# Performance work log

Hardware: AMD Instinct MI355X
Metric: run time of the kernel (lower is better)

Reference implementation:

```python
import jax, jax.numpy as jnp
import numpy as np

N, C = 32768, 1230   # batch of samples, LVIS-scale class count
P = 0.8              # seesaw scale parameter
EPS = 1e-6


def setup_inputs() -> dict:
    key = jax.random.key(0)
    k1, k2, k3 = jax.random.split(key, 3)
    logits = jax.random.normal(k1, (N, C), dtype=jnp.float32)
    labels = jax.random.randint(k2, (N,), 0, C)
    targets = jax.nn.one_hot(labels, C, dtype=jnp.float32)  # one-hot float targets
    # class_counts: long-tailed per-class sample counts (buffer, built in __init__)
    counts = jax.random.randint(k3, (C,), 1, 100000).astype(jnp.float32)
    cond = counts[:, None] > counts[None, :]
    s = jnp.where(cond, (counts[None, :] / counts[:, None]) ** P,
                  jnp.ones((C, C), dtype=jnp.float32))
    return {"logits": logits, "targets": targets, "s": s}


def reference(logits, targets, s):
    # numerically-stable shift (matches torch: logits - max)
    logits = logits - jnp.max(logits, axis=-1, keepdims=True)
    e = jnp.exp(logits)                                   # [N, C]
    # denom[n,i] = sum_j (1 - t[n,j]) * s[i,j] * e[n,j] + e[n,i]
    # original code materializes [N, C, C]; algebraically this is a GEMM:
    denom = jnp.einsum('nj,ij->ni', (1.0 - targets) * e, s) + e
    sigma = e / (denom + EPS)
    loss = -(targets * jnp.log(sigma)).sum(-1)            # [N]
    return loss.mean()
```

## Files before the change

kernel.cpp:

```cpp
#include <hip/hip_runtime.h>
#include <math.h>


constexpr int N_ROWS = 32768;
constexpr int C_CLS  = 1230;
constexpr int C2     = C_CLS / 2;
constexpr int BLK    = 256;
constexpr int WPB    = BLK / 64;
constexpr int ITERS  = (C2 + 63) / 64;
constexpr float EPS_F = 1e-6f;

__global__ __launch_bounds__(BLK) void seesaw_row_kernel(
    const float* __restrict__ logits,
    const float* __restrict__ targets,
    const float* __restrict__ s,
    float* __restrict__ row_loss)
{
    const int t    = threadIdx.x;
    const int lane = t & 63;
    const int wv   = t >> 6;
    const int n    = blockIdx.x * WPB + wv;

    const float2* lrow = reinterpret_cast<const float2*>(logits  + (size_t)n * C_CLS);
    const float2* trow = reinterpret_cast<const float2*>(targets + (size_t)n * C_CLS);

    float2 l[ITERS];
    float lmax = -INFINITY;
    float lval = 0.0f;
    int   li   = 0;

    #pragma unroll
    for (int it = 0; it < ITERS; ++it) {
        const int j2 = lane + it * 64;
        if (j2 < C2) {
            l[it] = lrow[j2];
            const float2 tv = trow[j2];
            lmax = fmaxf(lmax, fmaxf(l[it].x, l[it].y));
            if (tv.x > 0.5f) { li = 2 * j2;     lval = l[it].x; }
            if (tv.y > 0.5f) { li = 2 * j2 + 1; lval = l[it].y; }
        }
    }
    #pragma unroll
    for (int off = 32; off > 0; off >>= 1) {
        lmax  = fmaxf(lmax, __shfl_xor(lmax, off));
        li   += __shfl_xor(li, off);
        lval += __shfl_xor(lval, off);
    }
    const int   li_u = __builtin_amdgcn_readfirstlane(li);
    const float m    = lmax;

    const float2* srow = reinterpret_cast<const float2*>(s + (size_t)li_u * C_CLS);
    const float sii = s[(size_t)li_u * C_CLS + li_u];

    float part = 0.0f;
    #pragma unroll
    for (int it = 0; it < ITERS; ++it) {
        const int j2 = lane + it * 64;
        if (j2 < C2) {
            const float2 sv = srow[j2];
            part = fmaf(sv.x, __expf(l[it].x - m), part);
            part = fmaf(sv.y, __expf(l[it].y - m), part);
        }
    }
    #pragma unroll
    for (int off = 32; off > 0; off >>= 1)
        part += __shfl_xor(part, off);

    if (lane == 0) {
        const float ei    = __expf(lval - m);
        const float denom = part - sii * ei + ei;
        row_loss[n] = __logf(denom + EPS_F) - (lval - m);
    }
}

__global__ __launch_bounds__(BLK) void reduce_mean_kernel(
    const float* __restrict__ row_loss, float* __restrict__ out)
{
    const int t    = threadIdx.x;
    const int lane = t & 63;
    const int wv   = t >> 6;
    const float4* rl4 = reinterpret_cast<const float4*>(row_loss);
    constexpr int N4 = N_ROWS / 4;
    double acc = 0.0;
    #pragma unroll 4
    for (int i = t; i < N4; i += BLK) {
        const float4 v = rl4[i];
        acc += (double)v.x + (double)v.y + (double)v.z + (double)v.w;
    }
    #pragma unroll
    for (int off = 32; off > 0; off >>= 1)
        acc += __shfl_down(acc, off);
    __shared__ double red[4];
    if (lane == 0) red[wv] = acc;
    __syncthreads();
    if (t == 0) {
        const double tot = red[0] + red[1] + red[2] + red[3];
        out[0] = (float)(tot / (double)N_ROWS);
    }
}

extern "C" void kernel_launch(void* const* d_in, const int* in_sizes, int n_in,
                              void* d_out, int out_size, void* d_ws, size_t ws_size,
                              hipStream_t stream) {
    const float* logits  = (const float*)d_in[0];
    const float* targets = (const float*)d_in[1];
    const float* s       = (const float*)d_in[2];
    float* out      = (float*)d_out;
    float* row_loss = (float*)d_ws;

    seesaw_row_kernel<<<N_ROWS / WPB, BLK, 0, stream>>>(logits, targets, s, row_loss);
    reduce_mean_kernel<<<1, BLK, 0, stream>>>(row_loss, out);
}
```

Baseline: 330.4 us.

## Extract labels in a separate streaming pass and prefetch s rows alongside logits

```diff
diff --git a/kernel.cpp b/kernel.cpp
--- a/kernel.cpp
+++ b/kernel.cpp
@@ -8,12 +8,37 @@
 constexpr int BLK    = 256;
 constexpr int WPB    = BLK / 64;
 constexpr int ITERS  = (C2 + 63) / 64;
+constexpr unsigned TOT  = (unsigned)N_ROWS * (unsigned)C_CLS;
+constexpr unsigned TOT4 = TOT / 4;
 constexpr float EPS_F = 1e-6f;
+
+__global__ __launch_bounds__(BLK) void label_kernel(
+    const float* __restrict__ targets, int* __restrict__ labels)
+{
+    const float4* t4 = reinterpret_cast<const float4*>(targets);
+    const unsigned stride = gridDim.x * BLK;
+    for (unsigned i = blockIdx.x * BLK + threadIdx.x; i < TOT4; i += stride) {
+        const float4 v = t4[i];
+        if (v.x > 0.5f || v.y > 0.5f || v.z > 0.5f || v.w > 0.5f) {
+            const unsigned g = i * 4u;
+            #pragma unroll
+            for (int e = 0; e < 4; ++e) {
+                const float val = (e == 0) ? v.x : (e == 1) ? v.y : (e == 2) ? v.z : v.w;
+                if (val > 0.5f) {
+                    const unsigned gg = g + (unsigned)e;
+                    const unsigned n  = gg / (unsigned)C_CLS;
+                    const unsigned c  = gg - n * (unsigned)C_CLS;
+                    labels[n] = (int)c;
+                }
+            }
+        }
+    }
+}
 
 __global__ __launch_bounds__(BLK) void seesaw_row_kernel(
     const float* __restrict__ logits,
-    const float* __restrict__ targets,
     const float* __restrict__ s,
+    const int*   __restrict__ labels,
     float* __restrict__ row_loss)
 {
     const int t    = threadIdx.x;
@@ -21,45 +46,46 @@
     const int wv   = t >> 6;
     const int n    = blockIdx.x * WPB + wv;
 
-    const float2* lrow = reinterpret_cast<const float2*>(logits  + (size_t)n * C_CLS);
-    const float2* trow = reinterpret_cast<const float2*>(targets + (size_t)n * C_CLS);
+    const int li = __builtin_amdgcn_readfirstlane(labels[n]);
 
+    const float2* lrow = reinterpret_cast<const float2*>(logits + (size_t)n * C_CLS);
     float2 l[ITERS];
+    #pragma unroll
+    for (int it = 0; it < ITERS; ++it) {
+        const int j2  = lane + it * 64;
+        const int j2c = (j2 < C2) ? j2 : 0;
+        l[it] = lrow[j2c];
+    }
+
+    const float2* srow = reinterpret_cast<const float2*>(s + (size_t)li * C_CLS);
+    float2 sv[ITERS];
+    #pragma unroll
+    for (int it = 0; it < ITERS; ++it) {
+        const int j2  = lane + it * 64;
+        const int j2c = (j2 < C2) ? j2 : 0;
+        sv[it] = srow[j2c];
+    }
+    const float lval = logits[(size_t)n * C_CLS + li];
+    const float sii  = s[(size_t)li * C_CLS + li];
+
     float lmax = -INFINITY;
-    float lval = 0.0f;
-    int   li   = 0;
-
     #pragma unroll
     for (int it = 0; it < ITERS; ++it) {
         const int j2 = lane + it * 64;
-        if (j2 < C2) {
-            l[it] = lrow[j2];
-            const float2 tv = trow[j2];
-            lmax = fmaxf(lmax, fmaxf(l[it].x, l[it].y));
-            if (tv.x > 0.5f) { li = 2 * j2;     lval = l[it].x; }
-            if (tv.y > 0.5f) { li = 2 * j2 + 1; lval = l[it].y; }
-        }
+        if (j2 < C2) lmax = fmaxf(lmax, fmaxf(l[it].x, l[it].y));
     }
     #pragma unroll
-    for (int off = 32; off > 0; off >>= 1) {
-        lmax  = fmaxf(lmax, __shfl_xor(lmax, off));
-        li   += __shfl_xor(li, off);
-        lval += __shfl_xor(lval, off);
-    }
-    const int   li_u = __builtin_amdgcn_readfirstlane(li);
-    const float m    = lmax;
-
-    const float2* srow = reinterpret_cast<const float2*>(s + (size_t)li_u * C_CLS);
-    const float sii = s[(size_t)li_u * C_CLS + li_u];
+    for (int off = 32; off > 0; off >>= 1)
+        lmax = fmaxf(lmax, __shfl_xor(lmax, off));
+    const float m = lmax;
 
     float part = 0.0f;
     #pragma unroll
     for (int it = 0; it < ITERS; ++it) {
         const int j2 = lane + it * 64;
         if (j2 < C2) {
-            const float2 sv = srow[j2];
-            part = fmaf(sv.x, __expf(l[it].x - m), part);
-            part = fmaf(sv.y, __expf(l[it].y - m), part);
+            part = fmaf(sv[it].x, __expf(l[it].x - m), part);
+            part = fmaf(sv[it].y, __expf(l[it].y - m), part);
         }
     }
     #pragma unroll
@@ -73,7 +99,7 @@
     }
 }
 
-__global__ __launch_bounds__(BLK) void reduce_mean_kernel(
+__global__ __launch_bounds__(1024) void reduce_mean_kernel(
     const float* __restrict__ row_loss, float* __restrict__ out)
 {
     const int t    = threadIdx.x;
@@ -82,19 +108,21 @@
     const float4* rl4 = reinterpret_cast<const float4*>(row_loss);
     constexpr int N4 = N_ROWS / 4;
     double acc = 0.0;
-    #pragma unroll 4
-    for (int i = t; i < N4; i += BLK) {
+    #pragma unroll 8
+    for (int i = t; i < N4; i += 1024) {
         const float4 v = rl4[i];
         acc += (double)v.x + (double)v.y + (double)v.z + (double)v.w;
     }
     #pragma unroll
     for (int off = 32; off > 0; off >>= 1)
         acc += __shfl_down(acc, off);
-    __shared__ double red[4];
+    __shared__ double red[16];
     if (lane == 0) red[wv] = acc;
     __syncthreads();
     if (t == 0) {
-        const double tot = red[0] + red[1] + red[2] + red[3];
+        double tot = 0.0;
+        #pragma unroll
+        for (int w = 0; w < 16; ++w) tot += red[w];
         out[0] = (float)(tot / (double)N_ROWS);
     }
 }
@@ -105,9 +133,12 @@
     const float* logits  = (const float*)d_in[0];
     const float* targets = (const float*)d_in[1];
     const float* s       = (const float*)d_in[2];
-    float* out      = (float*)d_out;
-    float* row_loss = (float*)d_ws;
+    float* out = (float*)d_out;
 
-    seesaw_row_kernel<<<N_ROWS / WPB, BLK, 0, stream>>>(logits, targets, s, row_loss);
-    reduce_mean_kernel<<<1, BLK, 0, stream>>>(row_loss, out);
+    int*   labels   = (int*)d_ws;
+    float* row_loss = (float*)((char*)d_ws + N_ROWS * 4);
+
+    label_kernel<<<2048, BLK, 0, stream>>>(targets, labels);
+    seesaw_row_kernel<<<N_ROWS / WPB, BLK, 0, stream>>>(logits, s, labels, row_loss);
+    reduce_mean_kernel<<<1, 1024, 0, stream>>>(row_loss, out);
 }
```

New measurement: 323.5 us. -2.1%, faster.
